# Kernel tuning notes

Measured on AMD Instinct MI355X. Metric: run time of the kernel, lower is better.

The kernel has to match this reference:

```python
import jax, jax.numpy as jnp
import numpy as np

N, D, Z, T, K = 100000, 128, 128, 1024, 256
HID = 512
D_IN = D + 2 * Z  # concat of ctx, z_ctx_pe, z_tgt_pe


def setup_inputs() -> dict:
    key = jax.random.key(0)
    ks = jax.random.split(key, 12)
    inp = {
        'pe': jax.random.normal(ks[0], (N, 4), jnp.float32),
        'context_embedding': jax.random.normal(ks[1], (N, D), jnp.float32),
        'target_embedding': jax.random.normal(ks[2], (N, D), jnp.float32),
        # padded 2-hop subgraph node ids per target (precomputed k_hop_subgraph)
        'sub_nodes': jax.random.randint(ks[3], (T, K), 0, N, jnp.int32),
        'sub_counts': jax.random.randint(ks[4], (T,), 1, K + 1, jnp.int32),
        'target_nodes': jax.random.randint(ks[5], (T,), 0, N, jnp.int32),
        # params
        'z': jax.random.normal(ks[6], (1, Z), jnp.float32) * 0.1,
        'W_pe': jax.random.normal(ks[7], (4, Z), jnp.float32) * 0.5,
        'W1': jax.random.normal(ks[8], (D_IN, HID), jnp.float32) * (1.0 / np.sqrt(D_IN)),
        'b1': jnp.zeros((HID,), jnp.float32),
        'W2': jax.random.normal(ks[9], (HID, D), jnp.float32) * (1.0 / np.sqrt(HID)),
        'b2': jnp.zeros((D,), jnp.float32),
    }
    return inp


def reference(pe, context_embedding, target_embedding, sub_nodes, sub_counts,
              target_nodes, z, W_pe, W1, b1, W2, b2):
    # position_encoding = pe_projector(laplacian_eigenvector_pe)  [N, Z]
    pos_enc = pe @ W_pe
    # gather per-subgraph quantities (batched over T targets, padded to K)
    sub_ctx = context_embedding[sub_nodes]            # [T, K, D]
    z_ctx_pe = z + pos_enc[sub_nodes]                 # [T, K, Z]
    z_tgt_pe = z + pos_enc[target_nodes][:, None, :]  # [T, 1, Z] -> broadcast
    z_tgt_pe = jnp.broadcast_to(z_tgt_pe, z_ctx_pe.shape)
    agg = jnp.concatenate([sub_ctx, z_ctx_pe, z_tgt_pe], axis=-1)  # [T, K, D_IN]
    # predictor MLP
    pred = jax.nn.relu(agg @ W1 + b1) @ W2 + b2       # [T, K, D]
    tgt = target_embedding[target_nodes][:, None, :]  # [T, 1, D]
    sq = (pred - tgt) ** 2                            # [T, K, D]
    counts = jnp.maximum(sub_counts, 1)
    mask = (jnp.arange(K)[None, :] < counts[:, None]).astype(sq.dtype)  # [T, K]
    # per-target MSELoss (mean over n_sub * D elements), summed over targets
    per_target = jnp.sum(sq * mask[:, :, None], axis=(1, 2)) / (counts.astype(sq.dtype) * D)
    return jnp.sum(per_target)
```

## Files before the change

### kernel.cpp

```cpp
#include <hip/hip_runtime.h>
#include <hip/hip_bf16.h>

#define NN   100000
#define DD   128
#define ZZ   128
#define TT   1024
#define KK   256
#define HIDD 512

typedef __attribute__((ext_vector_type(8))) short  short8;
typedef __attribute__((ext_vector_type(4))) float  f32x4;

__device__ inline unsigned short f2bf(float f) {
    union { float f; unsigned int u; } x; x.f = f;
    unsigned int r = x.u + 0x7fffu + ((x.u >> 16) & 1u);
    return (unsigned short)(r >> 16);
}
__device__ inline float bf2f(unsigned short u) {
    union { unsigned int u; float f; } x; x.u = ((unsigned int)u) << 16;
    return x.f;
}
__device__ inline void load_lds16(const void* g, void* l) {
    __builtin_amdgcn_global_load_lds((const __attribute__((address_space(1))) unsigned int*)g,
                                     (__attribute__((address_space(3))) unsigned int*)l, 16, 0, 0);
}

__global__ __launch_bounds__(256) void prep_tables(
    const float* __restrict__ pe, const float* __restrict__ ctx,
    const float* __restrict__ z, const float* __restrict__ wpe,
    unsigned short* __restrict__ ctx_bf, unsigned short* __restrict__ zpe_bf) {
    int g = blockIdx.x * 256 + threadIdx.x;
    if (g >= NN * 16) return;
    int n = g >> 4, j8 = (g & 15) << 3;
    float p0 = pe[n * 4 + 0], p1 = pe[n * 4 + 1], p2 = pe[n * 4 + 2], p3 = pe[n * 4 + 3];
    float4 c0 = *(const float4*)(ctx + (size_t)n * 128 + j8);
    float4 c1 = *(const float4*)(ctx + (size_t)n * 128 + j8 + 4);
    float4 z0 = *(const float4*)(z + j8);
    float4 z1 = *(const float4*)(z + j8 + 4);
    float4 wa0 = *(const float4*)(wpe + 0 * ZZ + j8), wa1 = *(const float4*)(wpe + 0 * ZZ + j8 + 4);
    float4 wb0 = *(const float4*)(wpe + 1 * ZZ + j8), wb1 = *(const float4*)(wpe + 1 * ZZ + j8 + 4);
    float4 wc0 = *(const float4*)(wpe + 2 * ZZ + j8), wc1 = *(const float4*)(wpe + 2 * ZZ + j8 + 4);
    float4 wd0 = *(const float4*)(wpe + 3 * ZZ + j8), wd1 = *(const float4*)(wpe + 3 * ZZ + j8 + 4);
    float zp[8], cv[8];
    zp[0] = z0.x + p0 * wa0.x + p1 * wb0.x + p2 * wc0.x + p3 * wd0.x;
    zp[1] = z0.y + p0 * wa0.y + p1 * wb0.y + p2 * wc0.y + p3 * wd0.y;
    zp[2] = z0.z + p0 * wa0.z + p1 * wb0.z + p2 * wc0.z + p3 * wd0.z;
    zp[3] = z0.w + p0 * wa0.w + p1 * wb0.w + p2 * wc0.w + p3 * wd0.w;
    zp[4] = z1.x + p0 * wa1.x + p1 * wb1.x + p2 * wc1.x + p3 * wd1.x;
    zp[5] = z1.y + p0 * wa1.y + p1 * wb1.y + p2 * wc1.y + p3 * wd1.y;
    zp[6] = z1.z + p0 * wa1.z + p1 * wb1.z + p2 * wc1.z + p3 * wd1.z;
    zp[7] = z1.w + p0 * wa1.w + p1 * wb1.w + p2 * wc1.w + p3 * wd1.w;
    cv[0] = c0.x; cv[1] = c0.y; cv[2] = c0.z; cv[3] = c0.w;
    cv[4] = c1.x; cv[5] = c1.y; cv[6] = c1.z; cv[7] = c1.w;
    short8 sz, sc;
#pragma unroll
    for (int i = 0; i < 8; ++i) { sz[i] = (short)f2bf(zp[i]); sc[i] = (short)f2bf(cv[i]); }
    *(short8*)(zpe_bf + (size_t)g * 8) = sz;
    *(short8*)(ctx_bf + (size_t)g * 8) = sc;
}

__global__ __launch_bounds__(256) void pack_w(
    const float* __restrict__ W1, const float* __restrict__ W2,
    unsigned short* __restrict__ w1p, unsigned short* __restrict__ w2p) {
    int g = blockIdx.x * 256 + threadIdx.x;
    if (g < 256 * HIDD) {
        int e = g & 7, l = (g >> 3) & 63, tile = g >> 9;
        int ntg = tile & 7, rem = tile >> 3;
        int kc = rem & 7, hc = rem >> 3;
        int k = kc * 32 + (l >> 4) * 8 + e;
        int n = hc * 128 + ntg * 16 + (l & 15);
        w1p[g] = f2bf(W1[(size_t)k * HIDD + n]);
    } else {
        int q = g - 256 * HIDD;
        if (q < HIDD * DD) {
            int e = q & 7, l = (q >> 3) & 63, tile = q >> 9;
            int ntg = tile & 7, kcg = tile >> 3;
            int k = kcg * 32 + (l >> 4) * 8 + e;
            int n = ntg * 16 + (l & 15);
            w2p[q] = f2bf(W2[(size_t)k * DD + n]);
        }
    }
}

__global__ __launch_bounds__(256) void ct_kernel(
    const unsigned short* __restrict__ zpe_bf, const int* __restrict__ target_nodes,
    const float* __restrict__ W1, const float* __restrict__ b1, float* __restrict__ ct_g) {
    __shared__ float zp[8][128];
    int b = blockIdx.x, tid = threadIdx.x;
#pragma unroll
    for (int q = 0; q < 4; ++q) {
        int idx = q * 256 + tid;
        int t8 = idx >> 7, zz = idx & 127;
        int tgt = target_nodes[b * 8 + t8];
        zp[t8][zz] = bf2f(zpe_bf[(size_t)tgt * 128 + zz]);
    }
    __syncthreads();
    int j0 = tid, j1 = tid + 256;
    float a0[8], a1[8];
    float bb0 = b1[j0], bb1 = b1[j1];
#pragma unroll
    for (int t8 = 0; t8 < 8; ++t8) { a0[t8] = bb0; a1[t8] = bb1; }
#pragma unroll 8
    for (int zz = 0; zz < 128; ++zz) {
        float w0 = W1[(size_t)(256 + zz) * HIDD + j0];
        float w1 = W1[(size_t)(256 + zz) * HIDD + j1];
#pragma unroll
        for (int t8 = 0; t8 < 8; ++t8) { a0[t8] += zp[t8][zz] * w0; a1[t8] += zp[t8][zz] * w1; }
    }
#pragma unroll
    for (int t8 = 0; t8 < 8; ++t8) {
        ct_g[(size_t)(b * 8 + t8) * HIDD + j0] = a0[t8];
        ct_g[(size_t)(b * 8 + t8) * HIDD + j1] = a1[t8];
    }
}

__global__ __launch_bounds__(256, 3) void mp_jepa_main(
    const unsigned short* __restrict__ ctx_bf,
    const unsigned short* __restrict__ zpe_bf,
    const unsigned short* __restrict__ w1p,
    const unsigned short* __restrict__ w2p,
    const float* __restrict__ ct_g,
    const float* __restrict__ target_embedding,
    const int* __restrict__ sub_nodes,
    const int* __restrict__ sub_counts,
    const int* __restrict__ target_nodes,
    const float* __restrict__ b2,
    float* __restrict__ out) {
    const int bid = blockIdx.x;
    const int t = bid >> 2, kt = bid & 3;
    const int k0 = kt * 64;
    int cnt = sub_counts[t]; if (cnt < 1) cnt = 1;
    if (k0 >= cnt) return;
    const int tgt = target_nodes[t];

    __shared__ __align__(16) unsigned short ctxT[64 * 128];
    __shared__ __align__(16) unsigned short zpeT[64 * 128];
    __shared__ __align__(16) unsigned short hT[64 * 128];
    __shared__ float cts[HIDD];
    __shared__ float tgte[DD];
    __shared__ float b2s[DD];
    __shared__ float red[4];

    const int tid = threadIdx.x;
    const int w = tid >> 6, l = tid & 63;
    const int lo = l & 15, hi = l >> 4;

    {
        const char* cc = (const char*)ctx_bf;
        const char* zc = (const char*)zpe_bf;
        const int base = t * KK + k0;
#pragma unroll
        for (int it = 0; it < 4; ++it) {
            int rgrp = it * 16 + (w << 2);
            int row  = rgrp + hi;
            int node = sub_nodes[base + row];
            int soff = (lo << 4) ^ ((row & 7) << 4);
            load_lds16(cc + (size_t)node * 256 + soff, (char*)ctxT + rgrp * 256);
            load_lds16(zc + (size_t)node * 256 + soff, (char*)zpeT + rgrp * 256);
        }
    }
    if (tid < 128) {
        tgte[tid] = target_embedding[(size_t)tgt * 128 + tid];
        b2s[tid]  = b2[tid];
    }
    cts[tid]       = ct_g[(size_t)t * HIDD + tid];
    cts[tid + 256] = ct_g[(size_t)t * HIDD + tid + 256];
    __syncthreads();

    const short8* w1v = (const short8*)w1p;
    const short8* w2v = (const short8*)w2p;

    f32x4 accP[4][2];
#pragma unroll
    for (int rg = 0; rg < 4; ++rg)
#pragma unroll
        for (int nt = 0; nt < 2; ++nt) accP[rg][nt] = (f32x4){0.f, 0.f, 0.f, 0.f};

    for (int hc = 0; hc < 4; ++hc) {
        f32x4 acc1[4][2];
#pragma unroll
        for (int nt = 0; nt < 2; ++nt) {
            float c = cts[(hc << 7) + (w << 5) + (nt << 4) + lo];
#pragma unroll
            for (int rg = 0; rg < 4; ++rg) acc1[rg][nt] = (f32x4){c, c, c, c};
        }
#pragma unroll
        for (int kc = 0; kc < 8; ++kc) {
            int fb = ((hc << 3) + kc) << 3;
            short8 bf0 = w1v[(fb + (w << 1) + 0) * 64 + l];
            short8 bf1 = w1v[(fb + (w << 1) + 1) * 64 + l];
            const unsigned short* src = (kc < 4) ? ctxT : zpeT;
            int cb = ((kc & 3) << 6) + (hi << 4);
            short8 a[4];
#pragma unroll
            for (int rg = 0; rg < 4; ++rg) {
                int row = (rg << 4) + lo;
                a[rg] = *(const short8*)(src + ((row * 256 + (cb ^ ((row & 7) << 4))) >> 1));
            }
#pragma unroll
            for (int rg = 0; rg < 4; ++rg) {
                acc1[rg][0] = __builtin_amdgcn_mfma_f32_16x16x32_bf16(a[rg], bf0, acc1[rg][0], 0, 0, 0);
                acc1[rg][1] = __builtin_amdgcn_mfma_f32_16x16x32_bf16(a[rg], bf1, acc1[rg][1], 0, 0, 0);
            }
        }

        __syncthreads();
#pragma unroll
        for (int nt = 0; nt < 2; ++nt) {
            int col2 = ((w << 5) + (nt << 4) + lo) << 1;
#pragma unroll
            for (int rg = 0; rg < 4; ++rg) {
#pragma unroll
                for (int r = 0; r < 4; ++r) {
                    int row = (rg << 4) + (hi << 2) + r;
                    float v = acc1[rg][nt][r];
                    v = v > 0.f ? v : 0.f;
                    hT[(row * 256 + (col2 ^ ((row & 0xC) << 3))) >> 1] = f2bf(v);
                }
            }
        }
        __syncthreads();

#pragma unroll
        for (int kc2 = 0; kc2 < 4; ++kc2) {
            int kcg = (hc << 2) + kc2;
            short8 bg0 = w2v[(((kcg << 3) + (w << 1) + 0)) * 64 + l];
            short8 bg1 = w2v[(((kcg << 3) + (w << 1) + 1)) * 64 + l];
            int cb = (kc2 << 6) + (hi << 4);
#pragma unroll
            for (int rg = 0; rg < 4; ++rg) {
                int row = (rg << 4) + lo;
                short8 a = *(const short8*)(hT + ((row * 256 + (cb ^ ((row & 0xC) << 3))) >> 1));
                accP[rg][0] = __builtin_amdgcn_mfma_f32_16x16x32_bf16(a, bg0, accP[rg][0], 0, 0, 0);
                accP[rg][1] = __builtin_amdgcn_mfma_f32_16x16x32_bf16(a, bg1, accP[rg][1], 0, 0, 0);
            }
        }
    }

    float s = 0.f;
#pragma unroll
    for (int nt = 0; nt < 2; ++nt) {
        int col = (w << 5) + (nt << 4) + lo;
        float bb = b2s[col] - tgte[col];
#pragma unroll
        for (int rg = 0; rg < 4; ++rg) {
#pragma unroll
            for (int r = 0; r < 4; ++r) {
                int row = (rg << 4) + (hi << 2) + r;
                float d = accP[rg][nt][r] + bb;
                if (k0 + row < cnt) s += d * d;
            }
        }
    }
#pragma unroll
    for (int off = 32; off > 0; off >>= 1) s += __shfl_xor(s, off, 64);
    if (l == 0) red[w] = s;
    __syncthreads();
    if (tid == 0) {
        float tot = (red[0] + red[1] + red[2] + red[3]) / ((float)cnt * 128.0f);
        atomicAdd(out, tot);
    }
}

extern "C" void kernel_launch(void* const* d_in, const int* in_sizes, int n_in,
                              void* d_out, int out_size, void* d_ws, size_t ws_size,
                              hipStream_t stream) {
    const float* pe           = (const float*)d_in[0];
    const float* ctx          = (const float*)d_in[1];
    const float* tgt_emb      = (const float*)d_in[2];
    const int*   sub_nodes    = (const int*)d_in[3];
    const int*   sub_counts   = (const int*)d_in[4];
    const int*   target_nodes = (const int*)d_in[5];
    const float* z            = (const float*)d_in[6];
    const float* wpe          = (const float*)d_in[7];
    const float* W1           = (const float*)d_in[8];
    const float* b1           = (const float*)d_in[9];
    const float* W2           = (const float*)d_in[10];
    const float* b2           = (const float*)d_in[11];
    float* out = (float*)d_out;

    char* ws = (char*)d_ws;
    unsigned short* ctx_bf = (unsigned short*)ws;
    unsigned short* zpe_bf = (unsigned short*)(ws + 25600000);
    unsigned short* w1p    = (unsigned short*)(ws + 51200000);
    unsigned short* w2p    = (unsigned short*)(ws + 51200000 + 262144);
    float*          ct_g   = (float*)(ws + 51200000 + 262144 + 131072);

    hipMemsetAsync(d_out, 0, sizeof(float), stream);
    prep_tables<<<(NN * 16 + 255) / 256, 256, 0, stream>>>(pe, ctx, z, wpe, ctx_bf, zpe_bf);
    pack_w<<<(256 * HIDD + HIDD * DD + 255) / 256, 256, 0, stream>>>(W1, W2, w1p, w2p);
    ct_kernel<<<TT / 8, 256, 0, stream>>>(zpe_bf, target_nodes, W1, b1, ct_g);
    mp_jepa_main<<<TT * 4, 256, 0, stream>>>(ctx_bf, zpe_bf, w1p, w2p, ct_g, tgt_emb,
                                             sub_nodes, sub_counts, target_nodes, b2, out);
}
```

Before: 270.8 us.

## Fuse weight packing with target-term kernel and swap MFMA operands in main

```diff
diff --git a/kernel.cpp b/kernel.cpp
--- a/kernel.cpp
+++ b/kernel.cpp
@@ -15,10 +15,6 @@
     union { float f; unsigned int u; } x; x.f = f;
     unsigned int r = x.u + 0x7fffu + ((x.u >> 16) & 1u);
     return (unsigned short)(r >> 16);
-}
-__device__ inline float bf2f(unsigned short u) {
-    union { unsigned int u; float f; } x; x.u = ((unsigned int)u) << 16;
-    return x.f;
 }
 __device__ inline void load_lds16(const void* g, void* l) {
     __builtin_amdgcn_global_load_lds((const __attribute__((address_space(1))) unsigned int*)g,
@@ -59,40 +55,40 @@
     *(short8*)(ctx_bf + (size_t)g * 8) = sc;
 }
 
-__global__ __launch_bounds__(256) void pack_w(
+__global__ __launch_bounds__(256) void pack_ct(
     const float* __restrict__ W1, const float* __restrict__ W2,
-    unsigned short* __restrict__ w1p, unsigned short* __restrict__ w2p) {
-    int g = blockIdx.x * 256 + threadIdx.x;
-    if (g < 256 * HIDD) {
-        int e = g & 7, l = (g >> 3) & 63, tile = g >> 9;
-        int ntg = tile & 7, rem = tile >> 3;
-        int kc = rem & 7, hc = rem >> 3;
-        int k = kc * 32 + (l >> 4) * 8 + e;
-        int n = hc * 128 + ntg * 16 + (l & 15);
-        w1p[g] = f2bf(W1[(size_t)k * HIDD + n]);
-    } else {
-        int q = g - 256 * HIDD;
-        if (q < HIDD * DD) {
+    const float* __restrict__ pe, const float* __restrict__ z, const float* __restrict__ wpe,
+    const int* __restrict__ target_nodes, const float* __restrict__ b1,
+    unsigned short* __restrict__ w1p, unsigned short* __restrict__ w2p, float* __restrict__ ct_g) {
+    __shared__ float zp[8][128];
+    int tid = threadIdx.x;
+    if (blockIdx.x < 768) {
+        int g = blockIdx.x * 256 + tid;
+        if (g < 256 * HIDD) {
+            int e = g & 7, l = (g >> 3) & 63, tile = g >> 9;
+            int ntg = tile & 7, rem = tile >> 3;
+            int kc = rem & 7, hc = rem >> 3;
+            int k = kc * 32 + (l >> 4) * 8 + e;
+            int n = hc * 128 + ntg * 16 + (l & 15);
+            w1p[g] = f2bf(W1[(size_t)k * HIDD + n]);
+        } else {
+            int q = g - 256 * HIDD;
             int e = q & 7, l = (q >> 3) & 63, tile = q >> 9;
             int ntg = tile & 7, kcg = tile >> 3;
             int k = kcg * 32 + (l >> 4) * 8 + e;
             int n = ntg * 16 + (l & 15);
             w2p[q] = f2bf(W2[(size_t)k * DD + n]);
         }
-    }
-}
-
-__global__ __launch_bounds__(256) void ct_kernel(
-    const unsigned short* __restrict__ zpe_bf, const int* __restrict__ target_nodes,
-    const float* __restrict__ W1, const float* __restrict__ b1, float* __restrict__ ct_g) {
-    __shared__ float zp[8][128];
-    int b = blockIdx.x, tid = threadIdx.x;
+        return;
+    }
+    int b = blockIdx.x - 768;
 #pragma unroll
     for (int q = 0; q < 4; ++q) {
         int idx = q * 256 + tid;
         int t8 = idx >> 7, zz = idx & 127;
         int tgt = target_nodes[b * 8 + t8];
-        zp[t8][zz] = bf2f(zpe_bf[(size_t)tgt * 128 + zz]);
+        zp[t8][zz] = z[zz] + pe[tgt * 4 + 0] * wpe[zz] + pe[tgt * 4 + 1] * wpe[128 + zz]
+                           + pe[tgt * 4 + 2] * wpe[256 + zz] + pe[tgt * 4 + 3] * wpe[384 + zz];
     }
     __syncthreads();
     int j0 = tid, j1 = tid + 256;
@@ -114,7 +110,7 @@
     }
 }
 
-__global__ __launch_bounds__(256, 3) void mp_jepa_main(
+__global__ __launch_bounds__(256) void mp_jepa_main(
     const unsigned short* __restrict__ ctx_bf,
     const unsigned short* __restrict__ zpe_bf,
     const unsigned short* __restrict__ w1p,
@@ -177,18 +173,21 @@
         for (int nt = 0; nt < 2; ++nt) accP[rg][nt] = (f32x4){0.f, 0.f, 0.f, 0.f};
 
     for (int hc = 0; hc < 4; ++hc) {
+        short8 wA[16];
+#pragma unroll
+        for (int i = 0; i < 16; ++i) {
+            int kc = i >> 1, nt = i & 1;
+            wA[i] = w1v[((((hc << 3) + kc) << 3) + (w << 1) + nt) * 64 + l];
+        }
         f32x4 acc1[4][2];
 #pragma unroll
         for (int nt = 0; nt < 2; ++nt) {
-            float c = cts[(hc << 7) + (w << 5) + (nt << 4) + lo];
-#pragma unroll
-            for (int rg = 0; rg < 4; ++rg) acc1[rg][nt] = (f32x4){c, c, c, c};
+            f32x4 cv = *(const f32x4*)&cts[(hc << 7) + (((w << 1) + nt) << 4) + (hi << 2)];
+#pragma unroll
+            for (int rg = 0; rg < 4; ++rg) acc1[rg][nt] = cv;
         }
 #pragma unroll
         for (int kc = 0; kc < 8; ++kc) {
-            int fb = ((hc << 3) + kc) << 3;
-            short8 bf0 = w1v[(fb + (w << 1) + 0) * 64 + l];
-            short8 bf1 = w1v[(fb + (w << 1) + 1) * 64 + l];
             const unsigned short* src = (kc < 4) ? ctxT : zpeT;
             int cb = ((kc & 3) << 6) + (hi << 4);
             short8 a[4];
@@ -199,40 +198,47 @@
             }
 #pragma unroll
             for (int rg = 0; rg < 4; ++rg) {
-                acc1[rg][0] = __builtin_amdgcn_mfma_f32_16x16x32_bf16(a[rg], bf0, acc1[rg][0], 0, 0, 0);
-                acc1[rg][1] = __builtin_amdgcn_mfma_f32_16x16x32_bf16(a[rg], bf1, acc1[rg][1], 0, 0, 0);
-            }
+                acc1[rg][0] = __builtin_amdgcn_mfma_f32_16x16x32_bf16(wA[(kc << 1) + 0], a[rg], acc1[rg][0], 0, 0, 0);
+                acc1[rg][1] = __builtin_amdgcn_mfma_f32_16x16x32_bf16(wA[(kc << 1) + 1], a[rg], acc1[rg][1], 0, 0, 0);
+            }
+        }
+
+        short8 wB[8];
+#pragma unroll
+        for (int i = 0; i < 8; ++i) {
+            int kc2 = i >> 1, nt = i & 1;
+            wB[i] = w2v[((((hc << 2) + kc2) << 3) + (w << 1) + nt) * 64 + l];
         }
 
         __syncthreads();
 #pragma unroll
         for (int nt = 0; nt < 2; ++nt) {
-            int col2 = ((w << 5) + (nt << 4) + lo) << 1;
-#pragma unroll
-            for (int rg = 0; rg < 4; ++rg) {
-#pragma unroll
-                for (int r = 0; r < 4; ++r) {
-                    int row = (rg << 4) + (hi << 2) + r;
-                    float v = acc1[rg][nt][r];
-                    v = v > 0.f ? v : 0.f;
-                    hT[(row * 256 + (col2 ^ ((row & 0xC) << 3))) >> 1] = f2bf(v);
-                }
-            }
-        }
-        __syncthreads();
-
-#pragma unroll
-        for (int kc2 = 0; kc2 < 4; ++kc2) {
-            int kcg = (hc << 2) + kc2;
-            short8 bg0 = w2v[(((kcg << 3) + (w << 1) + 0)) * 64 + l];
-            short8 bg1 = w2v[(((kcg << 3) + (w << 1) + 1)) * 64 + l];
-            int cb = (kc2 << 6) + (hi << 4);
+            int cbase = (((w << 1) + nt) << 5) + (hi << 3);
 #pragma unroll
             for (int rg = 0; rg < 4; ++rg) {
                 int row = (rg << 4) + lo;
-                short8 a = *(const short8*)(hT + ((row * 256 + (cb ^ ((row & 0xC) << 3))) >> 1));
-                accP[rg][0] = __builtin_amdgcn_mfma_f32_16x16x32_bf16(a, bg0, accP[rg][0], 0, 0, 0);
-                accP[rg][1] = __builtin_amdgcn_mfma_f32_16x16x32_bf16(a, bg1, accP[rg][1], 0, 0, 0);
+                f32x4 v = acc1[rg][nt];
+                float v0 = v[0] > 0.f ? v[0] : 0.f;
+                float v1 = v[1] > 0.f ? v[1] : 0.f;
+                float v2 = v[2] > 0.f ? v[2] : 0.f;
+                float v3 = v[3] > 0.f ? v[3] : 0.f;
+                uint2 p;
+                p.x = (unsigned int)f2bf(v0) | ((unsigned int)f2bf(v1) << 16);
+                p.y = (unsigned int)f2bf(v2) | ((unsigned int)f2bf(v3) << 16);
+                *(uint2*)((char*)hT + row * 256 + (cbase ^ ((row & 7) << 4))) = p;
+            }
+        }
+        __syncthreads();
+
+#pragma unroll
+        for (int kc2 = 0; kc2 < 4; ++kc2) {
+            int cb = (kc2 << 6) + (hi << 4);
+#pragma unroll
+            for (int rg = 0; rg < 4; ++rg) {
+                int row = (rg << 4) + lo;
+                short8 a = *(const short8*)(hT + ((row * 256 + (cb ^ ((row & 7) << 4))) >> 1));
+                accP[rg][0] = __builtin_amdgcn_mfma_f32_16x16x32_bf16(a, wB[(kc2 << 1) + 0], accP[rg][0], 0, 0, 0);
+                accP[rg][1] = __builtin_amdgcn_mfma_f32_16x16x32_bf16(a, wB[(kc2 << 1) + 1], accP[rg][1], 0, 0, 0);
             }
         }
     }
@@ -288,8 +294,7 @@
 
     hipMemsetAsync(d_out, 0, sizeof(float), stream);
     prep_tables<<<(NN * 16 + 255) / 256, 256, 0, stream>>>(pe, ctx, z, wpe, ctx_bf, zpe_bf);
-    pack_w<<<(256 * HIDD + HIDD * DD + 255) / 256, 256, 0, stream>>>(W1, W2, w1p, w2p);
-    ct_kernel<<<TT / 8, 256, 0, stream>>>(zpe_bf, target_nodes, W1, b1, ct_g);
+    pack_ct<<<896, 256, 0, stream>>>(W1, W2, pe, z, wpe, target_nodes, b1, w1p, w2p, ct_g);
     mp_jepa_main<<<TT * 4, 256, 0, stream>>>(ctx_bf, zpe_bf, w1p, w2p, ct_g, tgt_emb,
                                              sub_nodes, sub_counts, target_nodes, b2, out);
 }
```

Measured after the change: 280.3 us. +3.5%, slower.
